# Performance work log

Hardware: AMD Instinct MI355X
Metric: run time of the kernel (lower is better)

The kernel has to match this reference:

```python
import jax, jax.numpy as jnp
import numpy as np

N = 50000        # nodes
E_RAND = 800000  # random edges (avg degree 16)
IN, HID, HEADS, OUT = 128, 32, 4, 64
NEG_SLOPE = 0.2  # PyG GATConv default leaky-relu slope


def setup_inputs() -> dict:
    key = jax.random.key(0)
    ks = jax.random.split(key, 12)
    x = jax.random.normal(ks[0], (N, IN), jnp.float32)
    src = jax.random.randint(ks[1], (E_RAND,), 0, N)
    dst = jax.random.randint(ks[2], (E_RAND,), 0, N)
    loop = jnp.arange(N)
    edge_src = jnp.concatenate([src, loop])  # self-loops, as PyG GATConv adds
    edge_dst = jnp.concatenate([dst, loop])
    g = lambda k, shape, fan: jax.random.normal(k, shape, jnp.float32) * np.float32(np.sqrt(2.0 / fan))
    W1 = g(ks[3], (IN, HEADS * HID), IN + HEADS * HID)
    att_src1 = g(ks[4], (HEADS, HID), HID)
    att_dst1 = g(ks[5], (HEADS, HID), HID)
    b1 = jnp.zeros((HEADS * HID,), jnp.float32)
    W2 = g(ks[6], (HEADS * HID, OUT), HEADS * HID + OUT)
    att_src2 = g(ks[7], (1, OUT), OUT)
    att_dst2 = g(ks[8], (1, OUT), OUT)
    b2 = jnp.zeros((OUT,), jnp.float32)
    return dict(x=x, edge_src=edge_src, edge_dst=edge_dst,
                W1=W1, att_src1=att_src1, att_dst1=att_dst1, b1=b1,
                W2=W2, att_src2=att_src2, att_dst2=att_dst2, b2=b2)


def gat_layer(x, src, dst, W, att_s, att_d, bias, heads, ch, concat):
    n = x.shape[0]
    h = (x @ W).reshape(n, heads, ch)                 # [N,H,C]
    a_s = (h * att_s).sum(-1)                          # [N,H]
    a_d = (h * att_d).sum(-1)                          # [N,H]
    e = jax.nn.leaky_relu(a_s[src] + a_d[dst], negative_slope=NEG_SLOPE)  # [E,H]
    # segment softmax over incoming edges per destination node
    m = jax.ops.segment_max(e, dst, num_segments=n)    # [N,H]
    ex = jnp.exp(e - m[dst])
    s = jax.ops.segment_sum(ex, dst, num_segments=n)
    alpha = ex / (s[dst] + 1e-16)                      # [E,H]
    out = jax.ops.segment_sum(alpha[:, :, None] * h[src], dst, num_segments=n)  # [N,H,C]
    out = out.reshape(n, heads * ch) if concat else out.mean(axis=1)
    return out + bias


def reference(x, edge_src, edge_dst, W1, att_src1, att_dst1, b1, W2, att_src2, att_dst2, b2):
    # dropout omitted: eval mode (training=False)
    h = jax.nn.relu(gat_layer(x, edge_src, edge_dst, W1, att_src1, att_dst1, b1, HEADS, HID, True))
    return gat_layer(h, edge_src, edge_dst, W2, att_src2, att_dst2, b2, 1, OUT, False)
```

## Files before the change

kernel.cpp:

```cpp
#include <hip/hip_runtime.h>
#include <hip/hip_bf16.h>
#include <cstring>


#define HEADS 4
#define HID   32
#define F1    128
#define F2    64
#define NEG   0.2f
#define EPB   1024
#define CAP   64

typedef __hip_bfloat16 bf16;
typedef unsigned short u16;
__device__ __forceinline__ float lrelu(float v) { return v > 0.f ? v : NEG * v; }
__device__ __forceinline__ float lo16(unsigned u) { return __uint_as_float(u << 16); }
__device__ __forceinline__ float hi16(unsigned u) { return __uint_as_float(u & 0xFFFF0000u); }

__global__ void k_curinit(int* __restrict__ cur, int N) {
    int i = blockIdx.x * blockDim.x + threadIdx.x;
    if (i < N) cur[i] = i * CAP;
}

__global__ void k_wsfail(unsigned* out_u, long nwords, unsigned w) {
    long i = blockIdx.x * (long)blockDim.x + threadIdx.x;
    if (i < nwords) out_u[i] = w;
}

__global__ void k_gemm1_scat(const float* __restrict__ x, const float* __restrict__ W,
                             const float* __restrict__ atts, const float* __restrict__ attd,
                             int N, bf16* __restrict__ h1,
                             float* __restrict__ as1, float* __restrict__ ad1,
                             const int* __restrict__ esrc, const int* __restrict__ edst,
                             int E, int* __restrict__ cur, u16* __restrict__ csr,
                             int S, int T) {
    __shared__ float xs[64][F1];
    int b = blockIdx.x;
    int s = (int)((long)b * S / T);
    int is_scat = ((long)(b + 1) * S / T) > (long)s;
    if (is_scat) {
        int base = s * EPB + threadIdx.x * 4;
        if (base + 3 < E) {
            int4 d4 = *(const int4*)(edst + base);
            int4 s4 = *(const int4*)(esrc + base);
            int p;
            p = atomicAdd(&cur[d4.x], 1); if (p < d4.x * CAP + CAP) csr[p] = (u16)s4.x;
            p = atomicAdd(&cur[d4.y], 1); if (p < d4.y * CAP + CAP) csr[p] = (u16)s4.y;
            p = atomicAdd(&cur[d4.z], 1); if (p < d4.z * CAP + CAP) csr[p] = (u16)s4.z;
            p = atomicAdd(&cur[d4.w], 1); if (p < d4.w * CAP + CAP) csr[p] = (u16)s4.w;
        } else {
            for (int i = base; i < E && i < base + 4; i++) {
                int d = edst[i];
                int p = atomicAdd(&cur[d], 1);
                if (p < d * CAP + CAP) csr[p] = (u16)esrc[i];
            }
        }
        return;
    }
    int g = b - s;
    int G = (N + 63) / 64;
    if (g >= G) return;
    int t = threadIdx.x;
    int nb = g * 64;
    for (int i = t; i < 64 * 32; i += 256) {
        int rr = i >> 5, c4 = i & 31;
        int n = nb + rr;
        float4 v = make_float4(0.f, 0.f, 0.f, 0.f);
        if (n < N) v = ((const float4*)(x + (size_t)n * F1))[c4];
        ((float4*)xs[rr])[c4] = v;
    }
    __syncthreads();
    int tc = t & 31, tr = t >> 5;
    int c0 = tc * 4;
    float acc[8][4] = {{0.f}};
    for (int k0 = 0; k0 < F1; k0 += 4) {
        #pragma unroll
        for (int kk = 0; kk < 4; kk++) {
            float4 wv = *(const float4*)&W[(size_t)(k0 + kk) * F1 + c0];
            #pragma unroll
            for (int i = 0; i < 8; i++) {
                float xv = xs[tr * 8 + i][k0 + kk];
                acc[i][0] += xv * wv.x;
                acc[i][1] += xv * wv.y;
                acc[i][2] += xv * wv.z;
                acc[i][3] += xv * wv.w;
            }
        }
    }
    #pragma unroll
    for (int i = 0; i < 8; i++) {
        int n = nb + tr * 8 + i;
        if (n < N) {
            union { bf16 b[4]; uint2 u; } pk;
            #pragma unroll
            for (int j = 0; j < 4; j++) pk.b[j] = __float2bfloat16(acc[i][j]);
            *(uint2*)(h1 + (size_t)n * F1 + c0) = pk.u;
        }
    }
    int hd = tc >> 3;
    float ps[8], pd[8];
    #pragma unroll
    for (int i = 0; i < 8; i++) {
        float s_ = 0.f, d_ = 0.f;
        #pragma unroll
        for (int j = 0; j < 4; j++) {
            s_ += acc[i][j] * atts[c0 + j];
            d_ += acc[i][j] * attd[c0 + j];
        }
        ps[i] = s_; pd[i] = d_;
    }
    #pragma unroll
    for (int off = 1; off < 8; off <<= 1) {
        #pragma unroll
        for (int i = 0; i < 8; i++) {
            ps[i] += __shfl_xor(ps[i], off);
            pd[i] += __shfl_xor(pd[i], off);
        }
    }
    if ((tc & 7) == 0) {
        #pragma unroll
        for (int i = 0; i < 8; i++) {
            int n = nb + tr * 8 + i;
            if (n < N) {
                as1[n * HEADS + hd] = ps[i];
                ad1[n * HEADS + hd] = pd[i];
            }
        }
    }
}

__global__ void k_agg1(const bf16* __restrict__ h1, const float* __restrict__ as1,
                       const float* __restrict__ ad1, const int* __restrict__ cur,
                       const u16* __restrict__ csr, const float* __restrict__ b1,
                       int N, float* __restrict__ feat) {
    int wave = threadIdx.x >> 6, lane = threadIdx.x & 63;
    int n = blockIdx.x * 4 + wave;
    if (n >= N) return;
    int r0 = n * CAP;
    int r1 = cur[n]; if (r1 > r0 + CAP) r1 = r0 + CAP;
    int sub = lane >> 4;
    int cl  = lane & 15;
    int head = cl >> 2;
    float adh = ad1[n * 4 + head];
    float acc[8] = {0.f, 0.f, 0.f, 0.f, 0.f, 0.f, 0.f, 0.f};
    float ssum = 0.f;
    int j0 = r0;
    for (; j0 + 12 < r1; j0 += 16) {
        int jA = j0 + sub, jB = j0 + 4 + sub, jC = j0 + 8 + sub, jD = j0 + 12 + sub;
        int vD = (jD < r1);
        int snA = csr[jA];
        int snB = csr[jB];
        int snC = csr[jC];
        int snD = vD ? csr[jD] : 0;
        float eA = as1[(size_t)snA * 4 + head];
        float eB = as1[(size_t)snB * 4 + head];
        float eC = as1[(size_t)snC * 4 + head];
        float eD = as1[(size_t)snD * 4 + head];
        const uint4 hvA = *(const uint4*)(h1 + (size_t)snA * F1 + cl * 8);
        const uint4 hvB = *(const uint4*)(h1 + (size_t)snB * F1 + cl * 8);
        const uint4 hvC = *(const uint4*)(h1 + (size_t)snC * F1 + cl * 8);
        const uint4 hvD = *(const uint4*)(h1 + (size_t)snD * F1 + cl * 8);
        float pA = __expf(lrelu(eA + adh));
        float pB = __expf(lrelu(eB + adh));
        float pC = __expf(lrelu(eC + adh));
        float pD = vD ? __expf(lrelu(eD + adh)) : 0.f;
        acc[0] += pA * lo16(hvA.x); acc[1] += pA * hi16(hvA.x);
        acc[2] += pA * lo16(hvA.y); acc[3] += pA * hi16(hvA.y);
        acc[4] += pA * lo16(hvA.z); acc[5] += pA * hi16(hvA.z);
        acc[6] += pA * lo16(hvA.w); acc[7] += pA * hi16(hvA.w);
        acc[0] += pB * lo16(hvB.x); acc[1] += pB * hi16(hvB.x);
        acc[2] += pB * lo16(hvB.y); acc[3] += pB * hi16(hvB.y);
        acc[4] += pB * lo16(hvB.z); acc[5] += pB * hi16(hvB.z);
        acc[6] += pB * lo16(hvB.w); acc[7] += pB * hi16(hvB.w);
        acc[0] += pC * lo16(hvC.x); acc[1] += pC * hi16(hvC.x);
        acc[2] += pC * lo16(hvC.y); acc[3] += pC * hi16(hvC.y);
        acc[4] += pC * lo16(hvC.z); acc[5] += pC * hi16(hvC.z);
        acc[6] += pC * lo16(hvC.w); acc[7] += pC * hi16(hvC.w);
        acc[0] += pD * lo16(hvD.x); acc[1] += pD * hi16(hvD.x);
        acc[2] += pD * lo16(hvD.y); acc[3] += pD * hi16(hvD.y);
        acc[4] += pD * lo16(hvD.z); acc[5] += pD * hi16(hvD.z);
        acc[6] += pD * lo16(hvD.w); acc[7] += pD * hi16(hvD.w);
        ssum += (pA + pB) + (pC + pD);
    }
    for (; j0 + 4 < r1; j0 += 8) {
        int jA = j0 + sub, jB = j0 + 4 + sub;
        int vB = (jB < r1);
        int snA = csr[jA];
        int snB = vB ? csr[jB] : 0;
        float eA = as1[(size_t)snA * 4 + head];
        float eB = as1[(size_t)snB * 4 + head];
        const uint4 hvA = *(const uint4*)(h1 + (size_t)snA * F1 + cl * 8);
        const uint4 hvB = *(const uint4*)(h1 + (size_t)snB * F1 + cl * 8);
        float pA = __expf(lrelu(eA + adh));
        float pB = vB ? __expf(lrelu(eB + adh)) : 0.f;
        acc[0] += pA * lo16(hvA.x); acc[1] += pA * hi16(hvA.x);
        acc[2] += pA * lo16(hvA.y); acc[3] += pA * hi16(hvA.y);
        acc[4] += pA * lo16(hvA.z); acc[5] += pA * hi16(hvA.z);
        acc[6] += pA * lo16(hvA.w); acc[7] += pA * hi16(hvA.w);
        acc[0] += pB * lo16(hvB.x); acc[1] += pB * hi16(hvB.x);
        acc[2] += pB * lo16(hvB.y); acc[3] += pB * hi16(hvB.y);
        acc[4] += pB * lo16(hvB.z); acc[5] += pB * hi16(hvB.z);
        acc[6] += pB * lo16(hvB.w); acc[7] += pB * hi16(hvB.w);
        ssum += pA + pB;
    }
    for (; j0 < r1; j0 += 4) {
        int j = j0 + sub;
        float p = 0.f;
        int sn = 0;
        if (j < r1) {
            sn = csr[j];
            p = __expf(lrelu(as1[(size_t)sn * 4 + head] + adh));
        }
        const uint4 hv = *(const uint4*)(h1 + (size_t)sn * F1 + cl * 8);
        acc[0] += p * lo16(hv.x); acc[1] += p * hi16(hv.x);
        acc[2] += p * lo16(hv.y); acc[3] += p * hi16(hv.y);
        acc[4] += p * lo16(hv.z); acc[5] += p * hi16(hv.z);
        acc[6] += p * lo16(hv.w); acc[7] += p * hi16(hv.w);
        ssum += p;
    }
    for (int off = 16; off < 64; off <<= 1) {
        ssum += __shfl_xor(ssum, off);
        #pragma unroll
        for (int k = 0; k < 8; k++) acc[k] += __shfl_xor(acc[k], off);
    }
    if (sub == 0) {
        float inv = 1.f / (ssum + 1e-16f);
        float* fp = feat + (size_t)n * F1 + cl * 8;
        #pragma unroll
        for (int k = 0; k < 8; k++) {
            float v = acc[k] * inv + b1[cl * 8 + k];
            fp[k] = v > 0.f ? v : 0.f;
        }
    }
}

__global__ void k_gemm2(const float* __restrict__ feat, const float* __restrict__ W,
                        const float* __restrict__ atts, const float* __restrict__ attd,
                        int N, bf16* __restrict__ h2,
                        float* __restrict__ as2, float* __restrict__ ad2) {
    __shared__ float fs[32][F1];
    int t = threadIdx.x;
    int nb = blockIdx.x * 32;
    for (int i = t; i < 32 * 32; i += 256) {
        int r = i >> 5, c4 = i & 31;
        int n = nb + r;
        float4 v = make_float4(0.f, 0.f, 0.f, 0.f);
        if (n < N) v = ((const float4*)(feat + (size_t)n * F1))[c4];
        ((float4*)fs[r])[c4] = v;
    }
    __syncthreads();
    int tc = t & 15, tr = t >> 4;
    int c0 = tc * 4;
    float acc[2][4] = {{0.f}};
    for (int k0 = 0; k0 < F1; k0 += 4) {
        float4 xr[2];
        #pragma unroll
        for (int i = 0; i < 2; i++)
            xr[i] = *(const float4*)&fs[tr * 2 + i][k0];
        #pragma unroll
        for (int kk = 0; kk < 4; kk++) {
            float4 wv = *(const float4*)&W[(size_t)(k0 + kk) * F2 + c0];
            #pragma unroll
            for (int i = 0; i < 2; i++) {
                float xv = ((const float*)(xr + i))[kk];
                acc[i][0] += xv * wv.x;
                acc[i][1] += xv * wv.y;
                acc[i][2] += xv * wv.z;
                acc[i][3] += xv * wv.w;
            }
        }
    }
    #pragma unroll
    for (int i = 0; i < 2; i++) {
        int n = nb + tr * 2 + i;
        if (n < N) {
            union { bf16 b[4]; uint2 u; } pk;
            #pragma unroll
            for (int j = 0; j < 4; j++) pk.b[j] = __float2bfloat16(acc[i][j]);
            *(uint2*)(h2 + (size_t)n * F2 + c0) = pk.u;
        }
    }
    float ps[2], pd[2];
    #pragma unroll
    for (int i = 0; i < 2; i++) {
        float s_ = 0.f, d_ = 0.f;
        #pragma unroll
        for (int j = 0; j < 4; j++) {
            s_ += acc[i][j] * atts[c0 + j];
            d_ += acc[i][j] * attd[c0 + j];
        }
        ps[i] = s_; pd[i] = d_;
    }
    #pragma unroll
    for (int off = 1; off < 16; off <<= 1) {
        #pragma unroll
        for (int i = 0; i < 2; i++) {
            ps[i] += __shfl_xor(ps[i], off);
            pd[i] += __shfl_xor(pd[i], off);
        }
    }
    if (tc == 0) {
        #pragma unroll
        for (int i = 0; i < 2; i++) {
            int n = nb + tr * 2 + i;
            if (n < N) { as2[n] = ps[i]; ad2[n] = pd[i]; }
        }
    }
}

__global__ void k_agg2(const bf16* __restrict__ h2, const float* __restrict__ as2,
                       const float* __restrict__ ad2, const int* __restrict__ cur,
                       const u16* __restrict__ csr, const float* __restrict__ b2v,
                       int N, float* __restrict__ out) {
    int wave = threadIdx.x >> 6, lane = threadIdx.x & 63;
    int n = blockIdx.x * 4 + wave;
    if (n >= N) return;
    int r0 = n * CAP;
    int r1 = cur[n]; if (r1 > r0 + CAP) r1 = r0 + CAP;
    int sub = lane >> 4;
    int cl  = lane & 15;
    float ad = ad2[n];
    float acc[4] = {0.f, 0.f, 0.f, 0.f};
    float ssum = 0.f;
    int j0 = r0;
    for (; j0 + 12 < r1; j0 += 16) {
        int jA = j0 + sub, jB = j0 + 4 + sub, jC = j0 + 8 + sub, jD = j0 + 12 + sub;
        int vD = (jD < r1);
        int snA = csr[jA];
        int snB = csr[jB];
        int snC = csr[jC];
        int snD = vD ? csr[jD] : 0;
        float eA = as2[snA];
        float eB = as2[snB];
        float eC = as2[snC];
        float eD = as2[snD];
        const uint2 hvA = *(const uint2*)(h2 + (size_t)snA * F2 + cl * 4);
        const uint2 hvB = *(const uint2*)(h2 + (size_t)snB * F2 + cl * 4);
        const uint2 hvC = *(const uint2*)(h2 + (size_t)snC * F2 + cl * 4);
        const uint2 hvD = *(const uint2*)(h2 + (size_t)snD * F2 + cl * 4);
        float pA = __expf(lrelu(eA + ad));
        float pB = __expf(lrelu(eB + ad));
        float pC = __expf(lrelu(eC + ad));
        float pD = vD ? __expf(lrelu(eD + ad)) : 0.f;
        acc[0] += pA * lo16(hvA.x); acc[1] += pA * hi16(hvA.x);
        acc[2] += pA * lo16(hvA.y); acc[3] += pA * hi16(hvA.y);
        acc[0] += pB * lo16(hvB.x); acc[1] += pB * hi16(hvB.x);
        acc[2] += pB * lo16(hvB.y); acc[3] += pB * hi16(hvB.y);
        acc[0] += pC * lo16(hvC.x); acc[1] += pC * hi16(hvC.x);
        acc[2] += pC * lo16(hvC.y); acc[3] += pC * hi16(hvC.y);
        acc[0] += pD * lo16(hvD.x); acc[1] += pD * hi16(hvD.x);
        acc[2] += pD * lo16(hvD.y); acc[3] += pD * hi16(hvD.y);
        ssum += (pA + pB) + (pC + pD);
    }
    for (; j0 + 4 < r1; j0 += 8) {
        int jA = j0 + sub, jB = j0 + 4 + sub;
        int vB = (jB < r1);
        int snA = csr[jA];
        int snB = vB ? csr[jB] : 0;
        float eA = as2[snA];
        float eB = as2[snB];
        const uint2 hvA = *(const uint2*)(h2 + (size_t)snA * F2 + cl * 4);
        const uint2 hvB = *(const uint2*)(h2 + (size_t)snB * F2 + cl * 4);
        float pA = __expf(lrelu(eA + ad));
        float pB = vB ? __expf(lrelu(eB + ad)) : 0.f;
        acc[0] += pA * lo16(hvA.x); acc[1] += pA * hi16(hvA.x);
        acc[2] += pA * lo16(hvA.y); acc[3] += pA * hi16(hvA.y);
        acc[0] += pB * lo16(hvB.x); acc[1] += pB * hi16(hvB.x);
        acc[2] += pB * lo16(hvB.y); acc[3] += pB * hi16(hvB.y);
        ssum += pA + pB;
    }
    for (; j0 < r1; j0 += 4) {
        int j = j0 + sub;
        float p = 0.f;
        int sn = 0;
        if (j < r1) {
            sn = csr[j];
            p = __expf(lrelu(as2[sn] + ad));
        }
        const uint2 hv = *(const uint2*)(h2 + (size_t)sn * F2 + cl * 4);
        acc[0] += p * lo16(hv.x); acc[1] += p * hi16(hv.x);
        acc[2] += p * lo16(hv.y); acc[3] += p * hi16(hv.y);
        ssum += p;
    }
    for (int off = 16; off < 64; off <<= 1) {
        ssum += __shfl_xor(ssum, off);
        #pragma unroll
        for (int k = 0; k < 4; k++) acc[k] += __shfl_xor(acc[k], off);
    }
    if (sub == 0) {
        float inv = 1.f / (ssum + 1e-16f);
        float* op = out + (size_t)n * F2 + cl * 4;
        #pragma unroll
        for (int k = 0; k < 4; k++) op[k] = acc[k] * inv + b2v[cl * 4 + k];
    }
}

extern "C" void kernel_launch(void* const* d_in, const int* in_sizes, int n_in,
                              void* d_out, int out_size, void* d_ws, size_t ws_size,
                              hipStream_t stream) {
    const float* x    = (const float*)d_in[0];
    const int* esrc   = (const int*)d_in[1];
    const int* edst   = (const int*)d_in[2];
    const float* W1   = (const float*)d_in[3];
    const float* at1s = (const float*)d_in[4];
    const float* at1d = (const float*)d_in[5];
    const float* b1   = (const float*)d_in[6];
    const float* W2   = (const float*)d_in[7];
    const float* at2s = (const float*)d_in[8];
    const float* at2d = (const float*)d_in[9];
    const float* b2   = (const float*)d_in[10];
    const int N = in_sizes[0] / F1;
    const int E = in_sizes[1];

    size_t off = 0;
    auto A = [&](size_t b) { size_t o = off; off = (off + b + 255) & ~(size_t)255; return o; };
    char* base = (char*)d_ws;
    size_t o_as1  = A((size_t)4 * N * 4);
    size_t o_ad1  = A((size_t)4 * N * 4);
    size_t o_h1   = A((size_t)N * F1 * 4);
    size_t o_feat = A((size_t)N * F1 * 4);
    size_t o_cur  = A((size_t)N * 4);
    size_t o_csr  = A((size_t)N * CAP * 2);
    size_t NEED = off;

    if (ws_size < NEED) {
        long nwords = (long)out_size;
        float val = 200.f;
        unsigned fb; memcpy(&fb, &val, 4);
        k_wsfail<<<(int)((nwords + 255) / 256), 256, 0, stream>>>(
            (unsigned*)d_out, nwords, fb);
        return;
    }

    float* as1  = (float*)(base + o_as1);
    float* ad1  = (float*)(base + o_ad1);
    float* as2  = as1;
    float* ad2  = ad1;
    bf16* h1    = (bf16*)(base + o_h1);
    bf16* h2    = h1;
    float* feat = (float*)(base + o_feat);
    int* cur    = (int*)(base + o_cur);
    u16* csr    = (u16*)(base + o_csr);

    k_curinit<<<(N + 255) / 256, 256, 0, stream>>>(cur, N);

    int G = (N + 63) / 64;
    int S = (E + EPB - 1) / EPB;
    int T = G + S;
    k_gemm1_scat<<<T, 256, 0, stream>>>(x, W1, at1s, at1d, N, h1, as1, ad1,
                                        esrc, edst, E, cur, csr, S, T);

    k_agg1<<<(N + 3) / 4, 256, 0, stream>>>(h1, as1, ad1, cur, csr, b1, N, feat);

    k_gemm2<<<(N + 31) / 32, 256, 0, stream>>>(feat, W2, at2s, at2d, N, h2, as2, ad2);
    k_agg2<<<(N + 3) / 4, 256, 0, stream>>>(h2, as2, ad2, cur, csr, b2, N, (float*)d_out);
}
```

Measured before the change: 236.2 us.

## Fuse layer-2 linear projection into layer-1 aggregation epilogue per wave

The layer-1 aggregation kernel now finishes its per-node features in registers (bias plus ReLU) and computes the 64-wide layer-2 projection and attention logits directly within the wave, using shuffles to broadcast features and reading W2 from global memory. This removes the separate GEMM2 launch and the fp32 feature round-trip through global memory. In exchange each wave does 128x64 FMAs with per-lane W2 loads (cached but not shared via LDS) and 128 shuffles. h2/as2/ad2 get dedicated buffers instead of aliasing h1/as1, since the fused kernel reads h1 while writing h2.

```diff
diff --git a/kernel.cpp b/kernel.cpp
--- a/kernel.cpp
+++ b/kernel.cpp
@@ -129,10 +129,13 @@
     }
 }
 
-__global__ void k_agg1(const bf16* __restrict__ h1, const float* __restrict__ as1,
-                       const float* __restrict__ ad1, const int* __restrict__ cur,
-                       const u16* __restrict__ csr, const float* __restrict__ b1,
-                       int N, float* __restrict__ feat) {
+__global__ void k_agg1g2(const bf16* __restrict__ h1, const float* __restrict__ as1,
+                         const float* __restrict__ ad1, const int* __restrict__ cur,
+                         const u16* __restrict__ csr, const float* __restrict__ b1,
+                         const float* __restrict__ W2, const float* __restrict__ at2s,
+                         const float* __restrict__ at2d,
+                         int N, bf16* __restrict__ h2,
+                         float* __restrict__ as2, float* __restrict__ ad2) {
     int wave = threadIdx.x >> 6, lane = threadIdx.x & 63;
     int n = blockIdx.x * 4 + wave;
     if (n >= N) return;
@@ -223,89 +226,30 @@
         #pragma unroll
         for (int k = 0; k < 8; k++) acc[k] += __shfl_xor(acc[k], off);
     }
-    if (sub == 0) {
-        float inv = 1.f / (ssum + 1e-16f);
-        float* fp = feat + (size_t)n * F1 + cl * 8;
-        #pragma unroll
-        for (int k = 0; k < 8; k++) {
-            float v = acc[k] * inv + b1[cl * 8 + k];
-            fp[k] = v > 0.f ? v : 0.f;
-        }
-    }
-}
-
-__global__ void k_gemm2(const float* __restrict__ feat, const float* __restrict__ W,
-                        const float* __restrict__ atts, const float* __restrict__ attd,
-                        int N, bf16* __restrict__ h2,
-                        float* __restrict__ as2, float* __restrict__ ad2) {
-    __shared__ float fs[32][F1];
-    int t = threadIdx.x;
-    int nb = blockIdx.x * 32;
-    for (int i = t; i < 32 * 32; i += 256) {
-        int r = i >> 5, c4 = i & 31;
-        int n = nb + r;
-        float4 v = make_float4(0.f, 0.f, 0.f, 0.f);
-        if (n < N) v = ((const float4*)(feat + (size_t)n * F1))[c4];
-        ((float4*)fs[r])[c4] = v;
-    }
-    __syncthreads();
-    int tc = t & 15, tr = t >> 4;
-    int c0 = tc * 4;
-    float acc[2][4] = {{0.f}};
-    for (int k0 = 0; k0 < F1; k0 += 4) {
-        float4 xr[2];
-        #pragma unroll
-        for (int i = 0; i < 2; i++)
-            xr[i] = *(const float4*)&fs[tr * 2 + i][k0];
-        #pragma unroll
-        for (int kk = 0; kk < 4; kk++) {
-            float4 wv = *(const float4*)&W[(size_t)(k0 + kk) * F2 + c0];
-            #pragma unroll
-            for (int i = 0; i < 2; i++) {
-                float xv = ((const float*)(xr + i))[kk];
-                acc[i][0] += xv * wv.x;
-                acc[i][1] += xv * wv.y;
-                acc[i][2] += xv * wv.z;
-                acc[i][3] += xv * wv.w;
-            }
-        }
-    }
+    float inv = 1.f / (ssum + 1e-16f);
+    float f[8];
     #pragma unroll
-    for (int i = 0; i < 2; i++) {
-        int n = nb + tr * 2 + i;
-        if (n < N) {
-            union { bf16 b[4]; uint2 u; } pk;
-            #pragma unroll
-            for (int j = 0; j < 4; j++) pk.b[j] = __float2bfloat16(acc[i][j]);
-            *(uint2*)(h2 + (size_t)n * F2 + c0) = pk.u;
-        }
-    }
-    float ps[2], pd[2];
+    for (int k = 0; k < 8; k++) {
+        float v = acc[k] * inv + b1[cl * 8 + k];
+        f[k] = v > 0.f ? v : 0.f;
+    }
+    float h2a = 0.f;
     #pragma unroll
-    for (int i = 0; i < 2; i++) {
-        float s_ = 0.f, d_ = 0.f;
-        #pragma unroll
-        for (int j = 0; j < 4; j++) {
-            s_ += acc[i][j] * atts[c0 + j];
-            d_ += acc[i][j] * attd[c0 + j];
-        }
-        ps[i] = s_; pd[i] = d_;
-    }
-    #pragma unroll
-    for (int off = 1; off < 16; off <<= 1) {
-        #pragma unroll
-        for (int i = 0; i < 2; i++) {
-            ps[i] += __shfl_xor(ps[i], off);
-            pd[i] += __shfl_xor(pd[i], off);
-        }
-    }
-    if (tc == 0) {
-        #pragma unroll
-        for (int i = 0; i < 2; i++) {
-            int n = nb + tr * 2 + i;
-            if (n < N) { as2[n] = ps[i]; ad2[n] = pd[i]; }
-        }
-    }
+    for (int cl2 = 0; cl2 < 16; cl2++) {
+        #pragma unroll
+        for (int j = 0; j < 8; j++) {
+            float fv = __shfl(f[j], cl2);
+            h2a += fv * W2[(size_t)(cl2 * 8 + j) * F2 + lane];
+        }
+    }
+    h2[(size_t)n * F2 + lane] = __float2bfloat16(h2a);
+    float s2 = h2a * at2s[lane];
+    float d2 = h2a * at2d[lane];
+    for (int off = 1; off < 64; off <<= 1) {
+        s2 += __shfl_xor(s2, off);
+        d2 += __shfl_xor(d2, off);
+    }
+    if (lane == 0) { as2[n] = s2; ad2[n] = d2; }
 }
 
 __global__ void k_agg2(const bf16* __restrict__ h2, const float* __restrict__ as2,
@@ -418,7 +362,9 @@
     size_t o_as1  = A((size_t)4 * N * 4);
     size_t o_ad1  = A((size_t)4 * N * 4);
     size_t o_h1   = A((size_t)N * F1 * 4);
-    size_t o_feat = A((size_t)N * F1 * 4);
+    size_t o_h2   = A((size_t)N * F2 * 2);
+    size_t o_as2  = A((size_t)N * 4);
+    size_t o_ad2  = A((size_t)N * 4);
     size_t o_cur  = A((size_t)N * 4);
     size_t o_csr  = A((size_t)N * CAP * 2);
     size_t NEED = off;
@@ -434,11 +380,10 @@
 
     float* as1  = (float*)(base + o_as1);
     float* ad1  = (float*)(base + o_ad1);
-    float* as2  = as1;
-    float* ad2  = ad1;
     bf16* h1    = (bf16*)(base + o_h1);
-    bf16* h2    = h1;
-    float* feat = (float*)(base + o_feat);
+    bf16* h2    = (bf16*)(base + o_h2);
+    float* as2  = (float*)(base + o_as2);
+    float* ad2  = (float*)(base + o_ad2);
     int* cur    = (int*)(base + o_cur);
     u16* csr    = (u16*)(base + o_csr);
 
@@ -450,8 +395,8 @@
     k_gemm1_scat<<<T, 256, 0, stream>>>(x, W1, at1s, at1d, N, h1, as1, ad1,
                                         esrc, edst, E, cur, csr, S, T);
 
-    k_agg1<<<(N + 3) / 4, 256, 0, stream>>>(h1, as1, ad1, cur, csr, b1, N, feat);
-
-    k_gemm2<<<(N + 31) / 32, 256, 0, stream>>>(feat, W2, at2s, at2d, N, h2, as2, ad2);
+    k_agg1g2<<<(N + 3) / 4, 256, 0, stream>>>(h1, as1, ad1, cur, csr, b1,
+                                              W2, at2s, at2d, N, h2, as2, ad2);
+
     k_agg2<<<(N + 3) / 4, 256, 0, stream>>>(h2, as2, ad2, cur, csr, b2, N, (float*)d_out);
 }
```

New measurement: 258.3 us. 1.09x slower.

## Split node features into 16-channel slices and aggregate each slice per block

Applied to the files above, without the earlier changes.

The GEMM kernels now write the bf16 node features as column slices of 16 channels, one N×16 array per slice, instead of row-major rows. The aggregation kernels launch one block group per slice, so each wave gathers only 32-byte pieces for 16 edges at a time. The aim is a smaller working set per slice pass, which should give better L2 hit rates on the random gathers and more parallel blocks. In exchange, the csr indices and attention scores are re-read once per slice, the loops are no longer unrolled, and h2, as2 and ad2 get their own workspace buffers instead of aliasing the layer-1 ones.

```diff
diff --git a/kernel.cpp b/kernel.cpp
--- a/kernel.cpp
+++ b/kernel.cpp
@@ -29,7 +29,7 @@
 
 __global__ void k_gemm1_scat(const float* __restrict__ x, const float* __restrict__ W,
                              const float* __restrict__ atts, const float* __restrict__ attd,
-                             int N, bf16* __restrict__ h1,
+                             int N, bf16* __restrict__ h1s,
                              float* __restrict__ as1, float* __restrict__ ad1,
                              const int* __restrict__ esrc, const int* __restrict__ edst,
                              int E, int* __restrict__ cur, u16* __restrict__ csr,
@@ -87,6 +87,7 @@
             }
         }
     }
+    size_t sl_base = (size_t)(tc >> 2) * N * 16 + (tc & 3) * 4;
     #pragma unroll
     for (int i = 0; i < 8; i++) {
         int n = nb + tr * 8 + i;
@@ -94,7 +95,7 @@
             union { bf16 b[4]; uint2 u; } pk;
             #pragma unroll
             for (int j = 0; j < 4; j++) pk.b[j] = __float2bfloat16(acc[i][j]);
-            *(uint2*)(h1 + (size_t)n * F1 + c0) = pk.u;
+            *(uint2*)(h1s + sl_base + (size_t)n * 16) = pk.u;
         }
     }
     int hd = tc >> 3;
@@ -129,106 +130,48 @@
     }
 }
 
-__global__ void k_agg1(const bf16* __restrict__ h1, const float* __restrict__ as1,
+__global__ void k_agg1(const bf16* __restrict__ h1s, const float* __restrict__ as1,
                        const float* __restrict__ ad1, const int* __restrict__ cur,
                        const u16* __restrict__ csr, const float* __restrict__ b1,
                        int N, float* __restrict__ feat) {
     int wave = threadIdx.x >> 6, lane = threadIdx.x & 63;
-    int n = blockIdx.x * 4 + wave;
+    int b = blockIdx.x;
+    int s = b & 7;
+    int n = (b >> 3) * 4 + wave;
     if (n >= N) return;
+    int head = s >> 1;
     int r0 = n * CAP;
     int r1 = cur[n]; if (r1 > r0 + CAP) r1 = r0 + CAP;
-    int sub = lane >> 4;
-    int cl  = lane & 15;
-    int head = cl >> 2;
+    int slot = lane >> 2, cl = lane & 3;
     float adh = ad1[n * 4 + head];
-    float acc[8] = {0.f, 0.f, 0.f, 0.f, 0.f, 0.f, 0.f, 0.f};
+    const bf16* hb = h1s + (size_t)s * N * 16 + cl * 4;
+    float acc[4] = {0.f, 0.f, 0.f, 0.f};
     float ssum = 0.f;
-    int j0 = r0;
-    for (; j0 + 12 < r1; j0 += 16) {
-        int jA = j0 + sub, jB = j0 + 4 + sub, jC = j0 + 8 + sub, jD = j0 + 12 + sub;
-        int vD = (jD < r1);
-        int snA = csr[jA];
-        int snB = csr[jB];
-        int snC = csr[jC];
-        int snD = vD ? csr[jD] : 0;
-        float eA = as1[(size_t)snA * 4 + head];
-        float eB = as1[(size_t)snB * 4 + head];
-        float eC = as1[(size_t)snC * 4 + head];
-        float eD = as1[(size_t)snD * 4 + head];
-        const uint4 hvA = *(const uint4*)(h1 + (size_t)snA * F1 + cl * 8);
-        const uint4 hvB = *(const uint4*)(h1 + (size_t)snB * F1 + cl * 8);
-        const uint4 hvC = *(const uint4*)(h1 + (size_t)snC * F1 + cl * 8);
-        const uint4 hvD = *(const uint4*)(h1 + (size_t)snD * F1 + cl * 8);
-        float pA = __expf(lrelu(eA + adh));
-        float pB = __expf(lrelu(eB + adh));
-        float pC = __expf(lrelu(eC + adh));
-        float pD = vD ? __expf(lrelu(eD + adh)) : 0.f;
-        acc[0] += pA * lo16(hvA.x); acc[1] += pA * hi16(hvA.x);
-        acc[2] += pA * lo16(hvA.y); acc[3] += pA * hi16(hvA.y);
-        acc[4] += pA * lo16(hvA.z); acc[5] += pA * hi16(hvA.z);
-        acc[6] += pA * lo16(hvA.w); acc[7] += pA * hi16(hvA.w);
-        acc[0] += pB * lo16(hvB.x); acc[1] += pB * hi16(hvB.x);
-        acc[2] += pB * lo16(hvB.y); acc[3] += pB * hi16(hvB.y);
-        acc[4] += pB * lo16(hvB.z); acc[5] += pB * hi16(hvB.z);
-        acc[6] += pB * lo16(hvB.w); acc[7] += pB * hi16(hvB.w);
-        acc[0] += pC * lo16(hvC.x); acc[1] += pC * hi16(hvC.x);
-        acc[2] += pC * lo16(hvC.y); acc[3] += pC * hi16(hvC.y);
-        acc[4] += pC * lo16(hvC.z); acc[5] += pC * hi16(hvC.z);
-        acc[6] += pC * lo16(hvC.w); acc[7] += pC * hi16(hvC.w);
-        acc[0] += pD * lo16(hvD.x); acc[1] += pD * hi16(hvD.x);
-        acc[2] += pD * lo16(hvD.y); acc[3] += pD * hi16(hvD.y);
-        acc[4] += pD * lo16(hvD.z); acc[5] += pD * hi16(hvD.z);
-        acc[6] += pD * lo16(hvD.w); acc[7] += pD * hi16(hvD.w);
-        ssum += (pA + pB) + (pC + pD);
-    }
-    for (; j0 + 4 < r1; j0 += 8) {
-        int jA = j0 + sub, jB = j0 + 4 + sub;
-        int vB = (jB < r1);
-        int snA = csr[jA];
-        int snB = vB ? csr[jB] : 0;
-        float eA = as1[(size_t)snA * 4 + head];
-        float eB = as1[(size_t)snB * 4 + head];
-        const uint4 hvA = *(const uint4*)(h1 + (size_t)snA * F1 + cl * 8);
-        const uint4 hvB = *(const uint4*)(h1 + (size_t)snB * F1 + cl * 8);
-        float pA = __expf(lrelu(eA + adh));
-        float pB = vB ? __expf(lrelu(eB + adh)) : 0.f;
-        acc[0] += pA * lo16(hvA.x); acc[1] += pA * hi16(hvA.x);
-        acc[2] += pA * lo16(hvA.y); acc[3] += pA * hi16(hvA.y);
-        acc[4] += pA * lo16(hvA.z); acc[5] += pA * hi16(hvA.z);
-        acc[6] += pA * lo16(hvA.w); acc[7] += pA * hi16(hvA.w);
-        acc[0] += pB * lo16(hvB.x); acc[1] += pB * hi16(hvB.x);
-        acc[2] += pB * lo16(hvB.y); acc[3] += pB * hi16(hvB.y);
-        acc[4] += pB * lo16(hvB.z); acc[5] += pB * hi16(hvB.z);
-        acc[6] += pB * lo16(hvB.w); acc[7] += pB * hi16(hvB.w);
-        ssum += pA + pB;
-    }
-    for (; j0 < r1; j0 += 4) {
-        int j = j0 + sub;
-        float p = 0.f;
-        int sn = 0;
-        if (j < r1) {
-            sn = csr[j];
-            p = __expf(lrelu(as1[(size_t)sn * 4 + head] + adh));
-        }
-        const uint4 hv = *(const uint4*)(h1 + (size_t)sn * F1 + cl * 8);
-        acc[0] += p * lo16(hv.x); acc[1] += p * hi16(hv.x);
-        acc[2] += p * lo16(hv.y); acc[3] += p * hi16(hv.y);
-        acc[4] += p * lo16(hv.z); acc[5] += p * hi16(hv.z);
-        acc[6] += p * lo16(hv.w); acc[7] += p * hi16(hv.w);
+    for (int j0 = r0; j0 < r1; j0 += 16) {
+        int j = j0 + slot;
+        int v = (j < r1);
+        int sn = v ? csr[j] : 0;
+        float e = as1[(size_t)sn * 4 + head];
+        const uint2 hv = *(const uint2*)(hb + (size_t)sn * 16);
+        float p = v ? __expf(lrelu(e + adh)) : 0.f;
+        acc[0] += p * lo16(hv.x);
+        acc[1] += p * hi16(hv.x);
+        acc[2] += p * lo16(hv.y);
+        acc[3] += p * hi16(hv.y);
         ssum += p;
     }
-    for (int off = 16; off < 64; off <<= 1) {
+    for (int off = 4; off < 64; off <<= 1) {
         ssum += __shfl_xor(ssum, off);
         #pragma unroll
-        for (int k = 0; k < 8; k++) acc[k] += __shfl_xor(acc[k], off);
-    }
-    if (sub == 0) {
+        for (int k = 0; k < 4; k++) acc[k] += __shfl_xor(acc[k], off);
+    }
+    if (slot == 0) {
         float inv = 1.f / (ssum + 1e-16f);
-        float* fp = feat + (size_t)n * F1 + cl * 8;
-        #pragma unroll
-        for (int k = 0; k < 8; k++) {
-            float v = acc[k] * inv + b1[cl * 8 + k];
+        int c0 = s * 16 + cl * 4;
+        float* fp = feat + (size_t)n * F1 + c0;
+        #pragma unroll
+        for (int k = 0; k < 4; k++) {
+            float v = acc[k] * inv + b1[c0 + k];
             fp[k] = v > 0.f ? v : 0.f;
         }
     }
@@ -236,7 +179,7 @@
 
 __global__ void k_gemm2(const float* __restrict__ feat, const float* __restrict__ W,
                         const float* __restrict__ atts, const float* __restrict__ attd,
-                        int N, bf16* __restrict__ h2,
+                        int N, bf16* __restrict__ h2s,
                         float* __restrict__ as2, float* __restrict__ ad2) {
     __shared__ float fs[32][F1];
     int t = threadIdx.x;
@@ -270,6 +213,7 @@
             }
         }
     }
+    size_t sl_base = (size_t)(tc >> 2) * N * 16 + (tc & 3) * 4;
     #pragma unroll
     for (int i = 0; i < 2; i++) {
         int n = nb + tr * 2 + i;
@@ -277,7 +221,7 @@
             union { bf16 b[4]; uint2 u; } pk;
             #pragma unroll
             for (int j = 0; j < 4; j++) pk.b[j] = __float2bfloat16(acc[i][j]);
-            *(uint2*)(h2 + (size_t)n * F2 + c0) = pk.u;
+            *(uint2*)(h2s + sl_base + (size_t)n * 16) = pk.u;
         }
     }
     float ps[2], pd[2];
@@ -308,90 +252,46 @@
     }
 }
 
-__global__ void k_agg2(const bf16* __restrict__ h2, const float* __restrict__ as2,
+__global__ void k_agg2(const bf16* __restrict__ h2s, const float* __restrict__ as2,
                        const float* __restrict__ ad2, const int* __restrict__ cur,
                        const u16* __restrict__ csr, const float* __restrict__ b2v,
                        int N, float* __restrict__ out) {
     int wave = threadIdx.x >> 6, lane = threadIdx.x & 63;
-    int n = blockIdx.x * 4 + wave;
+    int b = blockIdx.x;
+    int s = b & 3;
+    int n = (b >> 2) * 4 + wave;
     if (n >= N) return;
     int r0 = n * CAP;
     int r1 = cur[n]; if (r1 > r0 + CAP) r1 = r0 + CAP;
-    int sub = lane >> 4;
-    int cl  = lane & 15;
+    int slot = lane >> 2, cl = lane & 3;
     float ad = ad2[n];
+    const bf16* hb = h2s + (size_t)s * N * 16 + cl * 4;
     float acc[4] = {0.f, 0.f, 0.f, 0.f};
     float ssum = 0.f;
-    int j0 = r0;
-    for (; j0 + 12 < r1; j0 += 16) {
-        int jA = j0 + sub, jB = j0 + 4 + sub, jC = j0 + 8 + sub, jD = j0 + 12 + sub;
-        int vD = (jD < r1);
-        int snA = csr[jA];
-        int snB = csr[jB];
-        int snC = csr[jC];
-        int snD = vD ? csr[jD] : 0;
-        float eA = as2[snA];
-        float eB = as2[snB];
-        float eC = as2[snC];
-        float eD = as2[snD];
-        const uint2 hvA = *(const uint2*)(h2 + (size_t)snA * F2 + cl * 4);
-        const uint2 hvB = *(const uint2*)(h2 + (size_t)snB * F2 + cl * 4);
-        const uint2 hvC = *(const uint2*)(h2 + (size_t)snC * F2 + cl * 4);
-        const uint2 hvD = *(const uint2*)(h2 + (size_t)snD * F2 + cl * 4);
-        float pA = __expf(lrelu(eA + ad));
-        float pB = __expf(lrelu(eB + ad));
-        float pC = __expf(lrelu(eC + ad));
-        float pD = vD ? __expf(lrelu(eD + ad)) : 0.f;
-        acc[0] += pA * lo16(hvA.x); acc[1] += pA * hi16(hvA.x);
-        acc[2] += pA * lo16(hvA.y); acc[3] += pA * hi16(hvA.y);
-        acc[0] += pB * lo16(hvB.x); acc[1] += pB * hi16(hvB.x);
-        acc[2] += pB * lo16(hvB.y); acc[3] += pB * hi16(hvB.y);
-        acc[0] += pC * lo16(hvC.x); acc[1] += pC * hi16(hvC.x);
-        acc[2] += pC * lo16(hvC.y); acc[3] += pC * hi16(hvC.y);
-        acc[0] += pD * lo16(hvD.x); acc[1] += pD * hi16(hvD.x);
-        acc[2] += pD * lo16(hvD.y); acc[3] += pD * hi16(hvD.y);
-        ssum += (pA + pB) + (pC + pD);
-    }
-    for (; j0 + 4 < r1; j0 += 8) {
-        int jA = j0 + sub, jB = j0 + 4 + sub;
-        int vB = (jB < r1);
-        int snA = csr[jA];
-        int snB = vB ? csr[jB] : 0;
-        float eA = as2[snA];
-        float eB = as2[snB];
-        const uint2 hvA = *(const uint2*)(h2 + (size_t)snA * F2 + cl * 4);
-        const uint2 hvB = *(const uint2*)(h2 + (size_t)snB * F2 + cl * 4);
-        float pA = __expf(lrelu(eA + ad));
-        float pB = vB ? __expf(lrelu(eB + ad)) : 0.f;
-        acc[0] += pA * lo16(hvA.x); acc[1] += pA * hi16(hvA.x);
-        acc[2] += pA * lo16(hvA.y); acc[3] += pA * hi16(hvA.y);
-        acc[0] += pB * lo16(hvB.x); acc[1] += pB * hi16(hvB.x);
-        acc[2] += pB * lo16(hvB.y); acc[3] += pB * hi16(hvB.y);
-        ssum += pA + pB;
-    }
-    for (; j0 < r1; j0 += 4) {
-        int j = j0 + sub;
-        float p = 0.f;
-        int sn = 0;
-        if (j < r1) {
-            sn = csr[j];
-            p = __expf(lrelu(as2[sn] + ad));
-        }
-        const uint2 hv = *(const uint2*)(h2 + (size_t)sn * F2 + cl * 4);
-        acc[0] += p * lo16(hv.x); acc[1] += p * hi16(hv.x);
-        acc[2] += p * lo16(hv.y); acc[3] += p * hi16(hv.y);
+    for (int j0 = r0; j0 < r1; j0 += 16) {
+        int j = j0 + slot;
+        int v = (j < r1);
+        int sn = v ? csr[j] : 0;
+        float e = as2[sn];
+        const uint2 hv = *(const uint2*)(hb + (size_t)sn * 16);
+        float p = v ? __expf(lrelu(e + ad)) : 0.f;
+        acc[0] += p * lo16(hv.x);
+        acc[1] += p * hi16(hv.x);
+        acc[2] += p * lo16(hv.y);
+        acc[3] += p * hi16(hv.y);
         ssum += p;
     }
-    for (int off = 16; off < 64; off <<= 1) {
+    for (int off = 4; off < 64; off <<= 1) {
         ssum += __shfl_xor(ssum, off);
         #pragma unroll
         for (int k = 0; k < 4; k++) acc[k] += __shfl_xor(acc[k], off);
     }
-    if (sub == 0) {
+    if (slot == 0) {
         float inv = 1.f / (ssum + 1e-16f);
-        float* op = out + (size_t)n * F2 + cl * 4;
-        #pragma unroll
-        for (int k = 0; k < 4; k++) op[k] = acc[k] * inv + b2v[cl * 4 + k];
+        int c0 = s * 16 + cl * 4;
+        float* op = out + (size_t)n * F2 + c0;
+        #pragma unroll
+        for (int k = 0; k < 4; k++) op[k] = acc[k] * inv + b2v[c0 + k];
     }
 }
 
@@ -417,8 +317,11 @@
     char* base = (char*)d_ws;
     size_t o_as1  = A((size_t)4 * N * 4);
     size_t o_ad1  = A((size_t)4 * N * 4);
-    size_t o_h1   = A((size_t)N * F1 * 4);
+    size_t o_h1   = A((size_t)N * F1 * 2);
     size_t o_feat = A((size_t)N * F1 * 4);
+    size_t o_h2   = A((size_t)N * F2 * 2);
+    size_t o_as2  = A((size_t)N * 4);
+    size_t o_ad2  = A((size_t)N * 4);
     size_t o_cur  = A((size_t)N * 4);
     size_t o_csr  = A((size_t)N * CAP * 2);
     size_t NEED = off;
@@ -434,11 +337,11 @@
 
     float* as1  = (float*)(base + o_as1);
     float* ad1  = (float*)(base + o_ad1);
-    float* as2  = as1;
-    float* ad2  = ad1;
-    bf16* h1    = (bf16*)(base + o_h1);
-    bf16* h2    = h1;
+    bf16* h1s   = (bf16*)(base + o_h1);
     float* feat = (float*)(base + o_feat);
+    bf16* h2s   = (bf16*)(base + o_h2);
+    float* as2  = (float*)(base + o_as2);
+    float* ad2  = (float*)(base + o_ad2);
     int* cur    = (int*)(base + o_cur);
     u16* csr    = (u16*)(base + o_csr);
 
@@ -447,11 +350,13 @@
     int G = (N + 63) / 64;
     int S = (E + EPB - 1) / EPB;
     int T = G + S;
-    k_gemm1_scat<<<T, 256, 0, stream>>>(x, W1, at1s, at1d, N, h1, as1, ad1,
+    k_gemm1_scat<<<T, 256, 0, stream>>>(x, W1, at1s, at1d, N, h1s, as1, ad1,
                                         esrc, edst, E, cur, csr, S, T);
 
-    k_agg1<<<(N + 3) / 4, 256, 0, stream>>>(h1, as1, ad1, cur, csr, b1, N, feat);
-
-    k_gemm2<<<(N + 31) / 32, 256, 0, stream>>>(feat, W2, at2s, at2d, N, h2, as2, ad2);
-    k_agg2<<<(N + 3) / 4, 256, 0, stream>>>(h2, as2, ad2, cur, csr, b2, N, (float*)d_out);
-}
+    int NG = (N + 3) / 4;
+    k_agg1<<<NG * 8, 256, 0, stream>>>(h1s, as1, ad1, cur, csr, b1, N, feat);
+
+    k_gemm2<<<(N + 31) / 32, 256, 0, stream>>>(feat, W2, at2s, at2d, N, h2s, as2, ad2);
+
+    k_agg2<<<NG * 4, 256, 0, stream>>>(h2s, as2, ad2, cur, csr, b2, N, (float*)d_out);
+}
```

After: 361.9 us. +53.2%, slower.

## Split layer-1 aggregation into alpha precompute and feature-sliced gather

Applied to the files above, without the earlier changes.

Layer-1 attention coefficients are now computed once per edge and head in a separate kernel and stored as normalized fp16 values. Aggregation then runs over 8 feature slices of 16 channels each, with h1 stored slice-major so each slice's gathered rows are 32 bytes and more of them can stay in cache. This targets the random gather traffic of the aggregation, at the cost of an extra kernel, extra alpha traffic, 8x the blocks that each re-read the CSR, and fp16 rounding of alpha.

```diff
diff --git a/kernel.cpp b/kernel.cpp
--- a/kernel.cpp
+++ b/kernel.cpp
@@ -1,5 +1,6 @@
 #include <hip/hip_runtime.h>
 #include <hip/hip_bf16.h>
+#include <hip/hip_fp16.h>
 #include <cstring>
 
 
@@ -29,7 +30,7 @@
 
 __global__ void k_gemm1_scat(const float* __restrict__ x, const float* __restrict__ W,
                              const float* __restrict__ atts, const float* __restrict__ attd,
-                             int N, bf16* __restrict__ h1,
+                             int N, bf16* __restrict__ h1s,
                              float* __restrict__ as1, float* __restrict__ ad1,
                              const int* __restrict__ esrc, const int* __restrict__ edst,
                              int E, int* __restrict__ cur, u16* __restrict__ csr,
@@ -87,6 +88,7 @@
             }
         }
     }
+    size_t sl_base = (size_t)(tc >> 2) * N * 16 + (tc & 3) * 4;
     #pragma unroll
     for (int i = 0; i < 8; i++) {
         int n = nb + tr * 8 + i;
@@ -94,7 +96,7 @@
             union { bf16 b[4]; uint2 u; } pk;
             #pragma unroll
             for (int j = 0; j < 4; j++) pk.b[j] = __float2bfloat16(acc[i][j]);
-            *(uint2*)(h1 + (size_t)n * F1 + c0) = pk.u;
+            *(uint2*)(h1s + sl_base + (size_t)n * 16) = pk.u;
         }
     }
     int hd = tc >> 3;
@@ -129,106 +131,76 @@
     }
 }
 
-__global__ void k_agg1(const bf16* __restrict__ h1, const float* __restrict__ as1,
-                       const float* __restrict__ ad1, const int* __restrict__ cur,
-                       const u16* __restrict__ csr, const float* __restrict__ b1,
-                       int N, float* __restrict__ feat) {
+__global__ void k_alpha(const float* __restrict__ as1, const float* __restrict__ ad1,
+                        const int* __restrict__ cur, const u16* __restrict__ csr,
+                        int N, __half* __restrict__ alphaP) {
     int wave = threadIdx.x >> 6, lane = threadIdx.x & 63;
     int n = blockIdx.x * 4 + wave;
     if (n >= N) return;
     int r0 = n * CAP;
     int r1 = cur[n]; if (r1 > r0 + CAP) r1 = r0 + CAP;
-    int sub = lane >> 4;
-    int cl  = lane & 15;
-    int head = cl >> 2;
+    int slot = lane >> 2, head = lane & 3;
     float adh = ad1[n * 4 + head];
-    float acc[8] = {0.f, 0.f, 0.f, 0.f, 0.f, 0.f, 0.f, 0.f};
+    float p[4];
+    int jv[4];
     float ssum = 0.f;
-    int j0 = r0;
-    for (; j0 + 12 < r1; j0 += 16) {
-        int jA = j0 + sub, jB = j0 + 4 + sub, jC = j0 + 8 + sub, jD = j0 + 12 + sub;
-        int vD = (jD < r1);
-        int snA = csr[jA];
-        int snB = csr[jB];
-        int snC = csr[jC];
-        int snD = vD ? csr[jD] : 0;
-        float eA = as1[(size_t)snA * 4 + head];
-        float eB = as1[(size_t)snB * 4 + head];
-        float eC = as1[(size_t)snC * 4 + head];
-        float eD = as1[(size_t)snD * 4 + head];
-        const uint4 hvA = *(const uint4*)(h1 + (size_t)snA * F1 + cl * 8);
-        const uint4 hvB = *(const uint4*)(h1 + (size_t)snB * F1 + cl * 8);
-        const uint4 hvC = *(const uint4*)(h1 + (size_t)snC * F1 + cl * 8);
-        const uint4 hvD = *(const uint4*)(h1 + (size_t)snD * F1 + cl * 8);
-        float pA = __expf(lrelu(eA + adh));
-        float pB = __expf(lrelu(eB + adh));
-        float pC = __expf(lrelu(eC + adh));
-        float pD = vD ? __expf(lrelu(eD + adh)) : 0.f;
-        acc[0] += pA * lo16(hvA.x); acc[1] += pA * hi16(hvA.x);
-        acc[2] += pA * lo16(hvA.y); acc[3] += pA * hi16(hvA.y);
-        acc[4] += pA * lo16(hvA.z); acc[5] += pA * hi16(hvA.z);
-        acc[6] += pA * lo16(hvA.w); acc[7] += pA * hi16(hvA.w);
-        acc[0] += pB * lo16(hvB.x); acc[1] += pB * hi16(hvB.x);
-        acc[2] += pB * lo16(hvB.y); acc[3] += pB * hi16(hvB.y);
-        acc[4] += pB * lo16(hvB.z); acc[5] += pB * hi16(hvB.z);
-        acc[6] += pB * lo16(hvB.w); acc[7] += pB * hi16(hvB.w);
-        acc[0] += pC * lo16(hvC.x); acc[1] += pC * hi16(hvC.x);
-        acc[2] += pC * lo16(hvC.y); acc[3] += pC * hi16(hvC.y);
-        acc[4] += pC * lo16(hvC.z); acc[5] += pC * hi16(hvC.z);
-        acc[6] += pC * lo16(hvC.w); acc[7] += pC * hi16(hvC.w);
-        acc[0] += pD * lo16(hvD.x); acc[1] += pD * hi16(hvD.x);
-        acc[2] += pD * lo16(hvD.y); acc[3] += pD * hi16(hvD.y);
-        acc[4] += pD * lo16(hvD.z); acc[5] += pD * hi16(hvD.z);
-        acc[6] += pD * lo16(hvD.w); acc[7] += pD * hi16(hvD.w);
-        ssum += (pA + pB) + (pC + pD);
-    }
-    for (; j0 + 4 < r1; j0 += 8) {
-        int jA = j0 + sub, jB = j0 + 4 + sub;
-        int vB = (jB < r1);
-        int snA = csr[jA];
-        int snB = vB ? csr[jB] : 0;
-        float eA = as1[(size_t)snA * 4 + head];
-        float eB = as1[(size_t)snB * 4 + head];
-        const uint4 hvA = *(const uint4*)(h1 + (size_t)snA * F1 + cl * 8);
-        const uint4 hvB = *(const uint4*)(h1 + (size_t)snB * F1 + cl * 8);
-        float pA = __expf(lrelu(eA + adh));
-        float pB = vB ? __expf(lrelu(eB + adh)) : 0.f;
-        acc[0] += pA * lo16(hvA.x); acc[1] += pA * hi16(hvA.x);
-        acc[2] += pA * lo16(hvA.y); acc[3] += pA * hi16(hvA.y);
-        acc[4] += pA * lo16(hvA.z); acc[5] += pA * hi16(hvA.z);
-        acc[6] += pA * lo16(hvA.w); acc[7] += pA * hi16(hvA.w);
-        acc[0] += pB * lo16(hvB.x); acc[1] += pB * hi16(hvB.x);
-        acc[2] += pB * lo16(hvB.y); acc[3] += pB * hi16(hvB.y);
-        acc[4] += pB * lo16(hvB.z); acc[5] += pB * hi16(hvB.z);
-        acc[6] += pB * lo16(hvB.w); acc[7] += pB * hi16(hvB.w);
-        ssum += pA + pB;
-    }
-    for (; j0 < r1; j0 += 4) {
-        int j = j0 + sub;
-        float p = 0.f;
-        int sn = 0;
-        if (j < r1) {
-            sn = csr[j];
-            p = __expf(lrelu(as1[(size_t)sn * 4 + head] + adh));
-        }
-        const uint4 hv = *(const uint4*)(h1 + (size_t)sn * F1 + cl * 8);
-        acc[0] += p * lo16(hv.x); acc[1] += p * hi16(hv.x);
-        acc[2] += p * lo16(hv.y); acc[3] += p * hi16(hv.y);
-        acc[4] += p * lo16(hv.z); acc[5] += p * hi16(hv.z);
-        acc[6] += p * lo16(hv.w); acc[7] += p * hi16(hv.w);
-        ssum += p;
-    }
-    for (int off = 16; off < 64; off <<= 1) {
-        ssum += __shfl_xor(ssum, off);
-        #pragma unroll
-        for (int k = 0; k < 8; k++) acc[k] += __shfl_xor(acc[k], off);
-    }
-    if (sub == 0) {
-        float inv = 1.f / (ssum + 1e-16f);
-        float* fp = feat + (size_t)n * F1 + cl * 8;
-        #pragma unroll
-        for (int k = 0; k < 8; k++) {
-            float v = acc[k] * inv + b1[cl * 8 + k];
+    #pragma unroll
+    for (int it = 0; it < 4; it++) {
+        int j = r0 + it * 16 + slot;
+        int v = (j < r1);
+        jv[it] = v ? j : -1;
+        int sn = v ? csr[j] : 0;
+        float e = as1[(size_t)sn * 4 + head];
+        float pp = v ? __expf(lrelu(e + adh)) : 0.f;
+        p[it] = pp;
+        ssum += pp;
+    }
+    for (int off = 4; off < 64; off <<= 1) ssum += __shfl_xor(ssum, off);
+    float inv = 1.f / (ssum + 1e-16f);
+    __half* ap = alphaP + (size_t)head * N * CAP;
+    #pragma unroll
+    for (int it = 0; it < 4; it++) {
+        if (jv[it] >= 0) ap[jv[it]] = __float2half(p[it] * inv);
+    }
+}
+
+__global__ void k_agg1(const bf16* __restrict__ h1s, const __half* __restrict__ alphaP,
+                       const int* __restrict__ cur, const u16* __restrict__ csr,
+                       const float* __restrict__ b1, int N, float* __restrict__ feat) {
+    int wave = threadIdx.x >> 6, lane = threadIdx.x & 63;
+    int b = blockIdx.x;
+    int s = b & 7;
+    int n = (b >> 3) * 4 + wave;
+    if (n >= N) return;
+    int head = s >> 1;
+    int r0 = n * CAP;
+    int r1 = cur[n]; if (r1 > r0 + CAP) r1 = r0 + CAP;
+    int slot = lane >> 2, cl = lane & 3;
+    const bf16* hb = h1s + (size_t)s * N * 16 + cl * 4;
+    const __half* ap = alphaP + (size_t)head * N * CAP;
+    float acc[4] = {0.f, 0.f, 0.f, 0.f};
+    for (int j0 = r0; j0 < r1; j0 += 16) {
+        int j = j0 + slot;
+        int v = (j < r1);
+        int jj = v ? j : r0;
+        int sn = csr[jj];
+        float a = v ? __half2float(ap[jj]) : 0.f;
+        const uint2 hv = *(const uint2*)(hb + (size_t)sn * 16);
+        acc[0] += a * lo16(hv.x);
+        acc[1] += a * hi16(hv.x);
+        acc[2] += a * lo16(hv.y);
+        acc[3] += a * hi16(hv.y);
+    }
+    for (int off = 4; off < 64; off <<= 1) {
+        #pragma unroll
+        for (int k = 0; k < 4; k++) acc[k] += __shfl_xor(acc[k], off);
+    }
+    if (slot == 0) {
+        int c0 = s * 16 + cl * 4;
+        float* fp = feat + (size_t)n * F1 + c0;
+        #pragma unroll
+        for (int k = 0; k < 4; k++) {
+            float v = acc[k] + b1[c0 + k];
             fp[k] = v > 0.f ? v : 0.f;
         }
     }
@@ -415,12 +387,15 @@
     size_t off = 0;
     auto A = [&](size_t b) { size_t o = off; off = (off + b + 255) & ~(size_t)255; return o; };
     char* base = (char*)d_ws;
-    size_t o_as1  = A((size_t)4 * N * 4);
-    size_t o_ad1  = A((size_t)4 * N * 4);
-    size_t o_h1   = A((size_t)N * F1 * 4);
-    size_t o_feat = A((size_t)N * F1 * 4);
-    size_t o_cur  = A((size_t)N * 4);
-    size_t o_csr  = A((size_t)N * CAP * 2);
+    size_t o_as1   = A((size_t)4 * N * 4);
+    size_t o_ad1   = A((size_t)4 * N * 4);
+    size_t o_h1    = A((size_t)N * F1 * 2);
+    size_t o_feat  = A((size_t)N * F1 * 4);
+    size_t o_alpha = A((size_t)4 * N * CAP * 2);
+    size_t o_as2   = A((size_t)N * 4);
+    size_t o_ad2   = A((size_t)N * 4);
+    size_t o_cur   = A((size_t)N * 4);
+    size_t o_csr   = A((size_t)N * CAP * 2);
     size_t NEED = off;
 
     if (ws_size < NEED) {
@@ -432,26 +407,31 @@
         return;
     }
 
-    float* as1  = (float*)(base + o_as1);
-    float* ad1  = (float*)(base + o_ad1);
-    float* as2  = as1;
-    float* ad2  = ad1;
-    bf16* h1    = (bf16*)(base + o_h1);
-    bf16* h2    = h1;
-    float* feat = (float*)(base + o_feat);
-    int* cur    = (int*)(base + o_cur);
-    u16* csr    = (u16*)(base + o_csr);
+    float* as1     = (float*)(base + o_as1);
+    float* ad1     = (float*)(base + o_ad1);
+    bf16* h1s      = (bf16*)(base + o_h1);
+    float* feat    = (float*)(base + o_feat);
+    __half* alphaP = (__half*)(base + o_alpha);
+    bf16* h2       = (bf16*)(base + o_alpha);
+    float* as2     = (float*)(base + o_as2);
+    float* ad2     = (float*)(base + o_ad2);
+    int* cur       = (int*)(base + o_cur);
+    u16* csr       = (u16*)(base + o_csr);
 
     k_curinit<<<(N + 255) / 256, 256, 0, stream>>>(cur, N);
 
     int G = (N + 63) / 64;
     int S = (E + EPB - 1) / EPB;
     int T = G + S;
-    k_gemm1_scat<<<T, 256, 0, stream>>>(x, W1, at1s, at1d, N, h1, as1, ad1,
+    k_gemm1_scat<<<T, 256, 0, stream>>>(x, W1, at1s, at1d, N, h1s, as1, ad1,
                                         esrc, edst, E, cur, csr, S, T);
 
-    k_agg1<<<(N + 3) / 4, 256, 0, stream>>>(h1, as1, ad1, cur, csr, b1, N, feat);
+    int NB = (N + 3) / 4;
+    k_alpha<<<NB, 256, 0, stream>>>(as1, ad1, cur, csr, N, alphaP);
+
+    k_agg1<<<NB * 8, 256, 0, stream>>>(h1s, alphaP, cur, csr, b1, N, feat);
 
     k_gemm2<<<(N + 31) / 32, 256, 0, stream>>>(feat, W2, at2s, at2d, N, h2, as2, ad2);
-    k_agg2<<<(N + 3) / 4, 256, 0, stream>>>(h2, as2, ad2, cur, csr, b2, N, (float*)d_out);
-}
+
+    k_agg2<<<NB, 256, 0, stream>>>(h2, as2, ad2, cur, csr, b2, N, (float*)d_out);
+}
```

After: 324.7 us. 1.38x slower.
